# Kernel tuning notes

Hardware: AMD Instinct MI355X
Metric: run time of the kernel (lower is better)

The kernel has to match this reference:

```python
import jax, jax.numpy as jnp
import numpy as np

H, W, C = 96, 96, 21
SIGMA_RGB = 3.0   # bilateral spatial sdims (as called in the original code)
SIGMA_XY = 64.0   # gaussian spatial sdims
SCHAN = 255.0     # bilateral color std
COMPAT = 10.0     # Potts compatibility weight (same for both kernels)
N_ITERS = 5


def _gauss_kernel(feats):
    # feats: [N, D] -> K[i,j] = exp(-0.5 * ||f_i - f_j||^2)
    sq = jnp.sum(feats * feats, axis=-1)
    d2 = sq[:, None] + sq[None, :] - 2.0 * (feats @ feats.T)
    return jnp.exp(-0.5 * jnp.maximum(d2, 0.0))


def setup_inputs() -> dict:
    key = jax.random.key(0)
    k1, k2, k3 = jax.random.split(key, 3)
    logits = jax.random.normal(k1, (1, C, H, W), dtype=jnp.float32)
    labels = jax.random.randint(k2, (1, H, W), 0, C, dtype=jnp.int32)
    image = jax.random.uniform(k3, (1, 3, H, W), dtype=jnp.float32) * 255.0
    return {"logits": logits, "labels": labels, "image": image, "num_classes": C}


def reference(logits, labels, image, num_classes):
    # unary potentials: U = -log_softmax(logits)
    logp = jax.nn.log_softmax(logits, axis=1)              # [1,C,H,W]
    U = (-logp)[0].reshape(num_classes, -1).T              # [N,C]

    # pixel features
    yy, xx = jnp.meshgrid(jnp.arange(H), jnp.arange(W), indexing="ij")
    pos = jnp.stack([yy, xx], axis=-1).reshape(-1, 2).astype(logits.dtype)  # [N,2]
    rgb = image[0].transpose(1, 2, 0).reshape(-1, 3)        # [N,3]

    # dense pairwise kernels (exact Gaussian / bilateral, self-connection removed)
    N = H * W
    eye = jnp.eye(N, dtype=logits.dtype)
    Kg = _gauss_kernel(pos / SIGMA_XY) - eye
    fb = jnp.concatenate([pos / SIGMA_RGB, rgb / SCHAN], axis=-1)
    Kb = _gauss_kernel(fb) - eye

    # mean-field inference, Potts compatibility mu(l,l') = [l != l']
    Q0 = jax.nn.softmax(-U, axis=1)                         # [N,C]

    def step(Q, _):
        msg = Kg @ Q + Kb @ Q                               # [N,C] filtered Q
        pair = COMPAT * (jnp.sum(msg, axis=1, keepdims=True) - msg)
        Q = jax.nn.softmax(-U - pair, axis=1)
        return Q, None

    Q, _ = jax.lax.scan(step, Q0, None, length=N_ITERS)
    pairwise = Q.T.reshape(1, num_classes, H, W)

    # cross entropy (mean over pixels)
    ce = -jnp.mean(jnp.take_along_axis(logp, labels[:, None].astype(jnp.int32), axis=1))

    return ce + pairwise                                    # broadcast, as in original
```

## Files before the change

### kernel.cpp

```cpp
#include <hip/hip_runtime.h>
#include <hip/hip_fp16.h>

#define HH 96
#define WW 96
#define CC 21
#define NN (HH*WW)
#define NBLK (NN/256)
#define STRIDE 24
#define ROWF (WW*STRIDE)
#define NRUN (NN/8)

typedef _Float16 f16x8 __attribute__((ext_vector_type(8)));
typedef float f32x4 __attribute__((ext_vector_type(4)));

union H8 { f16x8 v; __half2 h2[4]; };


__global__ __launch_bounds__(256) void k_setup(
    const float* __restrict__ logits, const int* __restrict__ labels,
    const float* __restrict__ image, float* __restrict__ U,
    float* __restrict__ Q0, _Float16* __restrict__ QTa,
    _Float16* __restrict__ QTb, float* __restrict__ gtab,
    float* __restrict__ partial) {
  const int t = threadIdx.x;
  const int i = blockIdx.x * 256 + t;
  const int qoff = (i >> 3) * 192 + (i & 7);

  float d[CC];
  float mx = -1e30f;
#pragma unroll
  for (int c = 0; c < CC; ++c) {
    d[c] = logits[c * NN + i];
    mx = fmaxf(mx, d[c]);
  }
  float s = 0.f;
#pragma unroll
  for (int c = 0; c < CC; ++c) { d[c] -= mx; s += __expf(d[c]); }
  const float lse = logf(s);
  const float inv = 1.f / s;
  const int lab = labels[i];
  float myU = 0.f;
#pragma unroll
  for (int c = 0; c < CC; ++c) {
    const float Uc = lse - d[c];
    const float q = __expf(d[c]) * inv;
    U[i * STRIDE + c] = Uc;
    Q0[i * STRIDE + c] = q;
    QTa[qoff + c * 8] = (_Float16)q;
    myU = (c == lab) ? Uc : myU;
  }
  const float rr = image[i] * (1.f / 255.f);
  const float rg = image[NN + i] * (1.f / 255.f);
  const float rb = image[2 * NN + i] * (1.f / 255.f);
  U[i * STRIDE + 21] = 0.f;
  U[i * STRIDE + 22] = 0.f;
  U[i * STRIDE + 23] = 0.f;
  Q0[i * STRIDE + 21] = rr;
  Q0[i * STRIDE + 22] = rg;
  Q0[i * STRIDE + 23] = rb;
  QTa[qoff + 21 * 8] = (_Float16)rr;
  QTa[qoff + 22 * 8] = (_Float16)rg;
  QTa[qoff + 23 * 8] = (_Float16)rb;
  QTb[qoff + 21 * 8] = (_Float16)rr;
  QTb[qoff + 22 * 8] = (_Float16)rg;
  QTb[qoff + 23 * 8] = (_Float16)rb;

  if (blockIdx.x == 0 && t < 96) {
    const float dv = (float)t * (1.f / 64.f);
    gtab[t] = __expf(-0.5f * dv * dv);
  }

  __shared__ float red[256];
  red[t] = myU;
  __syncthreads();
  for (int off = 128; off > 0; off >>= 1) {
    if (t < off) red[t] += red[t + off];
    __syncthreads();
  }
  if (t == 0) partial[blockIdx.x] = red[0];
}

__global__ __launch_bounds__(256) void k_gauss_y(
    const float* __restrict__ Qin, float* __restrict__ Gy,
    const float* __restrict__ gtab) {
  __shared__ float g[96];
  if (threadIdx.x < 96) g[threadIdx.x] = gtab[threadIdx.x];
  __syncthreads();
  const int idx = blockIdx.x * 256 + threadIdx.x;
  const int y = idx / ROWF;
  const int rem = idx - y * ROWF;
  const float* base = Qin + rem;
  float acc = 0.f;
#pragma unroll 8
  for (int yp = 0; yp < HH; ++yp)
    acc = fmaf(g[abs(y - yp)], base[yp * ROWF], acc);
  Gy[idx] = acc;
}

__global__ __launch_bounds__(512) void k_bilat(
    const float* __restrict__ U, const float* __restrict__ Qin,
    const float* __restrict__ Gy, const _Float16* __restrict__ QT,
    const float* __restrict__ gtab, float* __restrict__ Qout,
    _Float16* __restrict__ QTout) {
  __shared__ __half sytab[64];
  __shared__ __half2 sxtab[64];
  __shared__ float sgt[96];
  __shared__ float psum[8][16][24];

  const int tid = threadIdx.x;
  const int w = tid >> 6;
  const int l = tid & 63;
  const int g = l >> 4;
  const int q = l & 15;

  if (tid < 64) {
    const float dv = (float)(tid - 32);
    sytab[tid] = __float2half(__expf(dv * dv * (-1.f / 18.f)));
    const float dv1 = dv + 1.f;
    sxtab[tid] = __floats2half2_rn(__expf(dv * dv * (-1.f / 18.f)),
                                   __expf(dv1 * dv1 * (-1.f / 18.f)));
  } else if (tid < 160) {
    sgt[tid - 64] = gtab[tid - 64];
  }
  __syncthreads();

  const int tile = blockIdx.x;
  const int ty0 = (tile / 24) * 4;
  const int tx0 = (tile - (tile / 24) * 24) * 4;

  const int pr = q >> 2, pc = q & 3;
  const int yi = ty0 + pr, xi = tx0 + pc;
  const int ipix = yi * WW + xi;

  const float4 rown = *(const float4*)(Qin + ipix * STRIDE + 20);
  const __half2 ri_r = __float2half2_rn(rown.y);
  const __half2 ri_g = __float2half2_rn(rown.z);
  const __half2 ri_b = __float2half2_rn(rown.w);
  const __half2 mhalf = __floats2half2_rn(-0.5f, -0.5f);
  const __half hzero = __float2half(0.f);

  const int xs = tx0 - 16;
  const int xbase0 = (xs > 0 ? xs : 0) & ~7;
  const int rows0 = (w < 4) ? w * 5 : 20 + (w - 4) * 4;
  const int nrun = ((w < 4) ? 5 : 4) * 5;
  const int nck = (nrun + 3) >> 2;

  const int row2 = (16 + q > 23) ? 23 : 16 + q;

  f32x4 acc0 = {0.f, 0.f, 0.f, 0.f};
  f32x4 acc1 = {0.f, 0.f, 0.f, 0.f};

#pragma unroll 2
  for (int ck = 0; ck < 7; ++ck) {
    if (ck >= nck) break;
    const int r = ck * 4 + g;
    const int wr = r / 5;
    const int cs = r - wr * 5;
    const int yj = ty0 - 16 + rows0 + wr;
    const int xb = xbase0 + cs * 8;
    const bool ok = (r < nrun) & (yj >= 0) & (yj < HH) & (xb <= WW - 8);
    const int yc = min(max(yj, 0), HH - 1);
    const int xc = min(xb, WW - 8);
    const _Float16* base = QT + (yc * 12 + (xc >> 3)) * 192;

    H8 b1, b2, rj, gj, bj;
    b1.v = *(const f16x8*)(base + q * 8);
    b2.v = *(const f16x8*)(base + row2 * 8);
    rj.v = *(const f16x8*)(base + 21 * 8);
    gj.v = *(const f16x8*)(base + 22 * 8);
    bj.v = *(const f16x8*)(base + 23 * 8);

    const int dy = yj - yi;
    const int iy = min(max(dy + 32, 0), 63);
    const __half syv = ok ? sytab[iy] : hzero;
    const __half2 sy2 = __half2half2(syv);
    const int dx0 = xb - xi;
    const int ix0 = min(max(dx0 + 32, 0), 57);

    H8 af;
#pragma unroll
    for (int e2 = 0; e2 < 4; ++e2) {
      const __half2 sx2 = sxtab[ix0 + 2 * e2];
      const __half2 dr = __hsub2(rj.h2[e2], ri_r);
      const __half2 dg = __hsub2(gj.h2[e2], ri_g);
      const __half2 db = __hsub2(bj.h2[e2], ri_b);
      __half2 d2c = __hmul2(dr, dr);
      d2c = __hfma2(dg, dg, d2c);
      d2c = __hfma2(db, db, d2c);
      const __half2 ec = h2exp(__hmul2(d2c, mhalf));
      af.h2[e2] = __hmul2(__hmul2(sy2, sx2), ec);
    }
    acc0 = __builtin_amdgcn_mfma_f32_16x16x32_f16(af.v, b1.v, acc0, 0, 0, 0);
    acc1 = __builtin_amdgcn_mfma_f32_16x16x32_f16(af.v, b2.v, acc1, 0, 0, 0);
  }

#pragma unroll
  for (int reg = 0; reg < 4; ++reg) {
    psum[w][g * 4 + reg][q] = acc0[reg];
    if (q < 8) psum[w][g * 4 + reg][16 + q] = acc1[reg];
  }
  __syncthreads();

  const int half_ = l >> 5;
  const int cl = l & 31;
  const bool act = cl < CC;
  const int pix = w * 2 + half_;
  const int py = ty0 + (pix >> 2), px = tx0 + (pix & 3);
  const int ip = py * WW + px;
  float Qic = 0.f;
  if (cl < STRIDE) Qic = Qin[ip * STRIDE + cl];
  float tcv = 0.f, Uc = 0.f, Gc = 0.f;
  if (act) {
    tcv = psum[0][pix][cl] + psum[1][pix][cl] + psum[2][pix][cl] +
          psum[3][pix][cl] + psum[4][pix][cl] + psum[5][pix][cl] +
          psum[6][pix][cl] + psum[7][pix][cl];
    Uc = U[ip * STRIDE + cl];
    const float* grow = Gy + py * ROWF + cl;
#pragma unroll 8
    for (int xp = 0; xp < WW; ++xp)
      Gc = fmaf(sgt[abs(px - xp)], grow[xp * STRIDE], Gc);
  }
  const float contrib = act ? (tcv + Gc - 2.f * Qic) : 0.f;
  float tot = contrib;
#pragma unroll
  for (int off = 16; off >= 1; off >>= 1) tot += __shfl_xor(tot, off, 32);
  const float lc = act ? (-Uc - 10.f * (tot - contrib)) : -1e30f;
  float mxl = lc;
#pragma unroll
  for (int off = 16; off >= 1; off >>= 1)
    mxl = fmaxf(mxl, __shfl_xor(mxl, off, 32));
  const float e = act ? __expf(lc - mxl) : 0.f;
  float se = e;
#pragma unroll
  for (int off = 16; off >= 1; off >>= 1) se += __shfl_xor(se, off, 32);
  const float qnew = e / se;
  if (cl < STRIDE) Qout[ip * STRIDE + cl] = act ? qnew : Qic;
  if (act) QTout[(ip >> 3) * 192 + cl * 8 + (ip & 7)] = (_Float16)qnew;
}

__global__ __launch_bounds__(256) void k_out(
    const float* __restrict__ Q, const float* __restrict__ partial,
    float* __restrict__ out) {
  __shared__ float ces;
  if (threadIdx.x < 64) {
    float v = (threadIdx.x < NBLK) ? partial[threadIdx.x] : 0.f;
#pragma unroll
    for (int off = 32; off > 0; off >>= 1) v += __shfl_down(v, off);
    if (threadIdx.x == 0) ces = v * (1.f / (float)NN);
  }
  __syncthreads();
  const int idx = blockIdx.x * 256 + threadIdx.x;
  if (idx >= CC * NN) return;
  const int c = idx / NN;
  const int i = idx - c * NN;
  out[idx] = ces + Q[i * STRIDE + c];
}

extern "C" void kernel_launch(void* const* d_in, const int* in_sizes, int n_in,
                              void* d_out, int out_size, void* d_ws,
                              size_t ws_size, hipStream_t stream) {
  const float* logits = (const float*)d_in[0];
  const int* labels = (const int*)d_in[1];
  const float* image = (const float*)d_in[2];
  float* ws = (float*)d_ws;

  float* U = ws;
  float* Qa = U + NN * STRIDE;
  float* Qb = Qa + NN * STRIDE;
  float* Gy = Qb + NN * STRIDE;
  float* gtab = Gy + NN * STRIDE;
  float* partial = gtab + 96;
  float* cepad = partial + 64;
  _Float16* QTa = (_Float16*)(cepad + 64);
  _Float16* QTb = QTa + NRUN * 192;

  k_setup<<<NBLK, 256, 0, stream>>>(logits, labels, image, U, Qa, QTa, QTb,
                                    gtab, partial);

  const float* qi = Qa;
  float* qo = Qb;
  const _Float16* qti = QTa;
  _Float16* qto = QTb;
  const int gblk = NN * STRIDE / 256;
  for (int it = 0; it < 5; ++it) {
    k_gauss_y<<<gblk, 256, 0, stream>>>(qi, Gy, gtab);
    k_bilat<<<576, 512, 0, stream>>>(U, qi, Gy, qti, gtab, qo, qto);
    qi = qo;
    qo = (qo == Qb) ? Qa : Qb;
    const _Float16* tmp = qti;
    qti = qto;
    qto = (_Float16*)tmp;
  }

  k_out<<<(CC * NN + 255) / 256, 256, 0, stream>>>(qi, partial, (float*)d_out);
}
```

Measured before the change: 142.6 us.

## Fuse output write into last bilateral pass, rebalance runs, split FMA chains

On the final iteration the bilateral kernel now writes the transposed output with the cross-entropy scalar added, which removes the separate output kernel launch and its read of Q. The bilateral work split is rebalanced so each wave processes a contiguous span of 23 or 22 runs in a fully unrolled 6-step loop, instead of per-wave row groups with an early break. The Gaussian y and x convolution loops now use four independent accumulators to shorten the FMA dependency chains. Summation order changes slightly, and the last-iteration branch adds a uniform runtime flag.

```diff
diff --git a/kernel.cpp b/kernel.cpp
--- a/kernel.cpp
+++ b/kernel.cpp
@@ -90,22 +90,28 @@
   const int y = idx / ROWF;
   const int rem = idx - y * ROWF;
   const float* base = Qin + rem;
-  float acc = 0.f;
-#pragma unroll 8
-  for (int yp = 0; yp < HH; ++yp)
-    acc = fmaf(g[abs(y - yp)], base[yp * ROWF], acc);
-  Gy[idx] = acc;
+  float a0 = 0.f, a1 = 0.f, a2 = 0.f, a3 = 0.f;
+#pragma unroll 6
+  for (int yp = 0; yp < HH; yp += 4) {
+    a0 = fmaf(g[abs(y - yp)], base[yp * ROWF], a0);
+    a1 = fmaf(g[abs(y - yp - 1)], base[(yp + 1) * ROWF], a1);
+    a2 = fmaf(g[abs(y - yp - 2)], base[(yp + 2) * ROWF], a2);
+    a3 = fmaf(g[abs(y - yp - 3)], base[(yp + 3) * ROWF], a3);
+  }
+  Gy[idx] = (a0 + a1) + (a2 + a3);
 }
 
 __global__ __launch_bounds__(512) void k_bilat(
     const float* __restrict__ U, const float* __restrict__ Qin,
     const float* __restrict__ Gy, const _Float16* __restrict__ QT,
     const float* __restrict__ gtab, float* __restrict__ Qout,
-    _Float16* __restrict__ QTout) {
+    _Float16* __restrict__ QTout, const float* __restrict__ partial,
+    float* __restrict__ out, int last) {
   __shared__ __half sytab[64];
   __shared__ __half2 sxtab[64];
   __shared__ float sgt[96];
   __shared__ float psum[8][16][24];
+  __shared__ float sces;
 
   const int tid = threadIdx.x;
   const int w = tid >> 6;
@@ -119,6 +125,12 @@
     const float dv1 = dv + 1.f;
     sxtab[tid] = __floats2half2_rn(__expf(dv * dv * (-1.f / 18.f)),
                                    __expf(dv1 * dv1 * (-1.f / 18.f)));
+    if (last) {
+      float v = (tid < NBLK) ? partial[tid] : 0.f;
+#pragma unroll
+      for (int off = 32; off >= 1; off >>= 1) v += __shfl_xor(v, off, 64);
+      if (tid == 0) sces = v * (1.f / (float)NN);
+    }
   } else if (tid < 160) {
     sgt[tid - 64] = gtab[tid - 64];
   }
@@ -141,22 +153,21 @@
 
   const int xs = tx0 - 16;
   const int xbase0 = (xs > 0 ? xs : 0) & ~7;
-  const int rows0 = (w < 4) ? w * 5 : 20 + (w - 4) * 4;
-  const int nrun = ((w < 4) ? 5 : 4) * 5;
-  const int nck = (nrun + 3) >> 2;
+  const int rid0 = (w < 4) ? w * 23 : 92 + (w - 4) * 22;
+  const int nrun = (w < 4) ? 23 : 22;
 
   const int row2 = (16 + q > 23) ? 23 : 16 + q;
 
   f32x4 acc0 = {0.f, 0.f, 0.f, 0.f};
   f32x4 acc1 = {0.f, 0.f, 0.f, 0.f};
 
-#pragma unroll 2
-  for (int ck = 0; ck < 7; ++ck) {
-    if (ck >= nck) break;
+#pragma unroll
+  for (int ck = 0; ck < 6; ++ck) {
     const int r = ck * 4 + g;
-    const int wr = r / 5;
-    const int cs = r - wr * 5;
-    const int yj = ty0 - 16 + rows0 + wr;
+    const int rid = rid0 + r;
+    const int wr = rid / 5;
+    const int cs = rid - wr * 5;
+    const int yj = ty0 - 16 + wr;
     const int xb = xbase0 + cs * 8;
     const bool ok = (r < nrun) & (yj >= 0) & (yj < HH) & (xb <= WW - 8);
     const int yc = min(max(yj, 0), HH - 1);
@@ -216,9 +227,15 @@
           psum[6][pix][cl] + psum[7][pix][cl];
     Uc = U[ip * STRIDE + cl];
     const float* grow = Gy + py * ROWF + cl;
-#pragma unroll 8
-    for (int xp = 0; xp < WW; ++xp)
-      Gc = fmaf(sgt[abs(px - xp)], grow[xp * STRIDE], Gc);
+    float g0 = 0.f, g1 = 0.f, g2 = 0.f, g3 = 0.f;
+#pragma unroll 6
+    for (int xp = 0; xp < WW; xp += 4) {
+      g0 = fmaf(sgt[abs(px - xp)], grow[xp * STRIDE], g0);
+      g1 = fmaf(sgt[abs(px - xp - 1)], grow[(xp + 1) * STRIDE], g1);
+      g2 = fmaf(sgt[abs(px - xp - 2)], grow[(xp + 2) * STRIDE], g2);
+      g3 = fmaf(sgt[abs(px - xp - 3)], grow[(xp + 3) * STRIDE], g3);
+    }
+    Gc = (g0 + g1) + (g2 + g3);
   }
   const float contrib = act ? (tcv + Gc - 2.f * Qic) : 0.f;
   float tot = contrib;
@@ -234,26 +251,12 @@
 #pragma unroll
   for (int off = 16; off >= 1; off >>= 1) se += __shfl_xor(se, off, 32);
   const float qnew = e / se;
-  if (cl < STRIDE) Qout[ip * STRIDE + cl] = act ? qnew : Qic;
-  if (act) QTout[(ip >> 3) * 192 + cl * 8 + (ip & 7)] = (_Float16)qnew;
-}
-
-__global__ __launch_bounds__(256) void k_out(
-    const float* __restrict__ Q, const float* __restrict__ partial,
-    float* __restrict__ out) {
-  __shared__ float ces;
-  if (threadIdx.x < 64) {
-    float v = (threadIdx.x < NBLK) ? partial[threadIdx.x] : 0.f;
-#pragma unroll
-    for (int off = 32; off > 0; off >>= 1) v += __shfl_down(v, off);
-    if (threadIdx.x == 0) ces = v * (1.f / (float)NN);
-  }
-  __syncthreads();
-  const int idx = blockIdx.x * 256 + threadIdx.x;
-  if (idx >= CC * NN) return;
-  const int c = idx / NN;
-  const int i = idx - c * NN;
-  out[idx] = ces + Q[i * STRIDE + c];
+  if (last) {
+    if (act) out[cl * NN + ip] = sces + qnew;
+  } else {
+    if (cl < STRIDE) Qout[ip * STRIDE + cl] = act ? qnew : Qic;
+    if (act) QTout[(ip >> 3) * 192 + cl * 8 + (ip & 7)] = (_Float16)qnew;
+  }
 }
 
 extern "C" void kernel_launch(void* const* d_in, const int* in_sizes, int n_in,
@@ -284,13 +287,12 @@
   const int gblk = NN * STRIDE / 256;
   for (int it = 0; it < 5; ++it) {
     k_gauss_y<<<gblk, 256, 0, stream>>>(qi, Gy, gtab);
-    k_bilat<<<576, 512, 0, stream>>>(U, qi, Gy, qti, gtab, qo, qto);
+    k_bilat<<<576, 512, 0, stream>>>(U, qi, Gy, qti, gtab, qo, qto, partial,
+                                     (float*)d_out, it == 4);
     qi = qo;
     qo = (qo == Qb) ? Qa : Qb;
     const _Float16* tmp = qti;
     qti = qto;
     qto = (_Float16*)tmp;
   }
-
-  k_out<<<(CC * NN + 255) / 256, 256, 0, stream>>>(qi, partial, (float*)d_out);
-}
+}
```

Result: faster. 138.2 us (-3.0%).
